# Kernel optimization log

Measured on AMD Instinct MI355X. Metric: run time of the kernel, lower is better.

The kernel has to match this reference:

```python
import jax, jax.numpy as jnp
import numpy as np

N_NODES = 100000
N_EDGES = 1250000
CH = [64, 64, 64]


def setup_inputs() -> dict:
    key = jax.random.key(0)
    ks = jax.random.split(key, 12)
    inp = {
        "x": jax.random.normal(ks[0], (N_NODES, CH[0]), dtype=jnp.float32),
        "edge_index": jax.random.randint(ks[1], (2, N_EDGES), 0, N_NODES, dtype=jnp.int64),
    }
    # Per-layer SAGEConv params (PyG default: out = lin_l(mean_aggr) + lin_r(x), bias only on lin_l)
    # plus per-channel PReLU weight (torch default init 0.25).
    for i in range(2):
        cin, cout = CH[i], CH[i + 1]
        s = 1.0 / np.sqrt(cin)
        inp[f"w_l{i}"] = jax.random.uniform(ks[2 + 4 * i], (cin, cout), jnp.float32, -s, s)
        inp[f"b_l{i}"] = jax.random.uniform(ks[3 + 4 * i], (cout,), jnp.float32, -s, s)
        inp[f"w_r{i}"] = jax.random.uniform(ks[4 + 4 * i], (cin, cout), jnp.float32, -s, s)
        inp[f"a{i}"] = jnp.full((cout,), 0.25, dtype=jnp.float32)
    return inp


def _sage_prelu(x, src, dst, w_l, b_l, w_r, a):
    n = x.shape[0]
    # mean aggregation of source features at destination nodes
    agg = jax.ops.segment_sum(x[src], dst, num_segments=n)  # [N, Cin]
    cnt = jax.ops.segment_sum(jnp.ones_like(dst, dtype=x.dtype), dst, num_segments=n)
    agg = agg / jnp.maximum(cnt, 1.0)[:, None]
    h = agg @ w_l + b_l + x @ w_r  # [N, Cout]
    return jnp.where(h >= 0, h, a * h)  # channel-wise PReLU


def reference(x, edge_index, w_l0, b_l0, w_r0, a0, w_l1, b_l1, w_r1, a1):
    src, dst = edge_index[0], edge_index[1]
    h = _sage_prelu(x, src, dst, w_l0, b_l0, w_r0, a0)
    h = _sage_prelu(h, src, dst, w_l1, b_l1, w_r1, a1)
    return h
```

## Files before the change

kernel.cpp:

```cpp
#include <hip/hip_runtime.h>
#include <hip/hip_fp16.h>

#define N_NODES 100000
#define N_EDGES 1250000
#define C 64
#define NPB 128
#define NB 782
#define CAP 2048
#define P1_CHUNKQ 2048
#define P1_BLOCKS 153
#define NQ (N_EDGES / 4)

typedef int vint4 __attribute__((ext_vector_type(4)));

__global__ __launch_bounds__(256) void partition_kernel(
        const int* __restrict__ src, const int* __restrict__ dst,
        int* __restrict__ gcnt, unsigned int* __restrict__ packed) {
    __shared__ int s_hist[4][NB];
    __shared__ int s_cur[NB];
    const int t = threadIdx.x;
    const int w = t >> 6;
    for (int i = t; i < 4 * NB; i += 256) ((int*)s_hist)[i] = 0;
    __syncthreads();

    const int qbase = blockIdx.x * P1_CHUNKQ;
    const vint4* d4 = (const vint4*)dst;
    const vint4* s4 = (const vint4*)src;

    vint4 dreg[8], sreg[8];
    bool val[8];
#pragma unroll
    for (int k = 0; k < 8; ++k) {
        int q = qbase + k * 256 + t;
        val[k] = q < NQ;
        if (val[k]) {
            dreg[k] = __builtin_nontemporal_load(&d4[q]);
            sreg[k] = __builtin_nontemporal_load(&s4[q]);
        }
    }

#pragma unroll
    for (int k = 0; k < 8; ++k) {
        if (val[k]) {
            atomicAdd(&s_hist[w][dreg[k].x >> 7], 1);
            atomicAdd(&s_hist[w][dreg[k].y >> 7], 1);
            atomicAdd(&s_hist[w][dreg[k].z >> 7], 1);
            atomicAdd(&s_hist[w][dreg[k].w >> 7], 1);
        }
    }
    __syncthreads();

    for (int b = t; b < NB; b += 256) {
        int tot = s_hist[0][b] + s_hist[1][b] + s_hist[2][b] + s_hist[3][b];
        s_cur[b] = (tot > 0) ? (b * CAP + atomicAdd(&gcnt[b], tot)) : 0;
    }
    __syncthreads();

#pragma unroll
    for (int k = 0; k < 8; ++k) {
        if (val[k]) {
            int bb, pos;
            bb = dreg[k].x >> 7; pos = atomicAdd(&s_cur[bb], 1);
            if (pos < (bb + 1) * CAP) packed[pos] = ((unsigned)sreg[k].x << 7) | (unsigned)(dreg[k].x & 127);
            bb = dreg[k].y >> 7; pos = atomicAdd(&s_cur[bb], 1);
            if (pos < (bb + 1) * CAP) packed[pos] = ((unsigned)sreg[k].y << 7) | (unsigned)(dreg[k].y & 127);
            bb = dreg[k].z >> 7; pos = atomicAdd(&s_cur[bb], 1);
            if (pos < (bb + 1) * CAP) packed[pos] = ((unsigned)sreg[k].z << 7) | (unsigned)(dreg[k].z & 127);
            bb = dreg[k].w >> 7; pos = atomicAdd(&s_cur[bb], 1);
            if (pos < (bb + 1) * CAP) packed[pos] = ((unsigned)sreg[k].w << 7) | (unsigned)(dreg[k].w & 127);
        }
    }
}

__global__ __launch_bounds__(256) void sort_kernel(
        const unsigned int* __restrict__ packed,
        const int* __restrict__ gcnt,
        int* __restrict__ offsets, int* __restrict__ sorted_src) {
    __shared__ int s_part[256];
    __shared__ unsigned int s_e[CAP];
    __shared__ int s_hist[NPB];
    __shared__ int s_excl[NPB];
    const int b = blockIdx.x;
    const int t = threadIdx.x;

    int psum = 0;
    for (int i = t; i < b; i += 256) psum += gcnt[i];
    s_part[t] = psum;
    __syncthreads();
    for (int off = 128; off > 0; off >>= 1) {
        if (t < off) s_part[t] += s_part[t + off];
        __syncthreads();
    }
    const int base = s_part[0];
    const int nb = min(gcnt[b], CAP);

    for (int i = t; i < NPB; i += 256) s_hist[i] = 0;
    __syncthreads();
    const vint4* p4 = (const vint4*)(packed + (size_t)b * CAP);
    for (int i4 = t; i4 * 4 < nb; i4 += 256) {
        vint4 u4 = __builtin_nontemporal_load(&p4[i4]);
        int i = i4 * 4;
        unsigned int u;
        u = (unsigned)u4.x; if (i + 0 < nb) { s_e[i + 0] = u; atomicAdd(&s_hist[u & 127u], 1); }
        u = (unsigned)u4.y; if (i + 1 < nb) { s_e[i + 1] = u; atomicAdd(&s_hist[u & 127u], 1); }
        u = (unsigned)u4.z; if (i + 2 < nb) { s_e[i + 2] = u; atomicAdd(&s_hist[u & 127u], 1); }
        u = (unsigned)u4.w; if (i + 3 < nb) { s_e[i + 3] = u; atomicAdd(&s_hist[u & 127u], 1); }
    }
    __syncthreads();
    if (t < NPB) s_excl[t] = s_hist[t];
    __syncthreads();
    for (int off = 1; off < NPB; off <<= 1) {
        int v = (t < NPB && t >= off) ? s_excl[t - off] : 0;
        __syncthreads();
        if (t < NPB) s_excl[t] += v;
        __syncthreads();
    }
    if (t < NPB) {
        int excl = s_excl[t] - s_hist[t];
        s_hist[t] = excl;
        int node = b * NPB + t;
        if (node < N_NODES) offsets[node] = base + excl;
    }
    __syncthreads();
    for (int i = t; i < nb; i += 256) {
        unsigned int u = s_e[i];
        int lp = atomicAdd(&s_hist[u & 127u], 1);
        sorted_src[base + lp] = (int)(u >> 7);
    }
    if (b == NB - 1 && t == 0) offsets[N_NODES] = N_EDGES;
}

template <typename XT>
__global__ __launch_bounds__(256) void dense_kernel(
        const XT* __restrict__ x,
        const float* __restrict__ wl, const float* __restrict__ wr,
        const float* __restrict__ bl,
        __half* __restrict__ z, __half* __restrict__ r, int n_nodes) {
    __shared__ float s_w[C][2 * C];
    __shared__ float s_x[64][C + 1];

    const int t = threadIdx.x;
    const int base = blockIdx.x * 64;

    for (int i = t; i < C * C; i += 256) {
        int k = i >> 6, c = i & 63;
        s_w[k][c] = wl[i];
        s_w[k][64 + c] = wr[i];
    }
    if constexpr (sizeof(XT) == 4) {
        for (int i = t; i < 1024; i += 256) {
            int n = i >> 4;
            int kq = i & 15;
            float4 v = make_float4(0.f, 0.f, 0.f, 0.f);
            if (base + n < n_nodes) v = ((const float4*)x)[((size_t)(base + n) << 4) + kq];
            s_x[n][kq * 4 + 0] = v.x;
            s_x[n][kq * 4 + 1] = v.y;
            s_x[n][kq * 4 + 2] = v.z;
            s_x[n][kq * 4 + 3] = v.w;
        }
    } else {
        for (int i = t; i < 2048; i += 256) {
            int n = i >> 5;
            int c2 = i & 31;
            float2 f = make_float2(0.f, 0.f);
            if (base + n < n_nodes)
                f = __half22float2(((const __half2*)x)[(size_t)(base + n) * 32 + c2]);
            s_x[n][2 * c2 + 0] = f.x;
            s_x[n][2 * c2 + 1] = f.y;
        }
    }
    __syncthreads();

    const int lane = t & 63;
    const int wv = t >> 6;
    const int cg = lane & 15;
    const int q = lane >> 4;
    const int n0 = wv * 16 + 4 * q;

    float4 bv = ((const float4*)bl)[cg];
    float accz[4][4];
    float accr[4][4];
#pragma unroll
    for (int i = 0; i < 4; ++i) {
        accz[i][0] = accz[i][1] = accz[i][2] = accz[i][3] = 0.f;
        accr[i][0] = bv.x; accr[i][1] = bv.y; accr[i][2] = bv.z; accr[i][3] = bv.w;
    }

#pragma unroll 8
    for (int k = 0; k < C; ++k) {
        float4 wlv = *(const float4*)&s_w[k][4 * cg];
        float4 wrv = *(const float4*)&s_w[k][64 + 4 * cg];
        float xk[4];
#pragma unroll
        for (int i = 0; i < 4; ++i) xk[i] = s_x[n0 + i][k];
#pragma unroll
        for (int i = 0; i < 4; ++i) {
            accz[i][0] += xk[i] * wlv.x;
            accz[i][1] += xk[i] * wlv.y;
            accz[i][2] += xk[i] * wlv.z;
            accz[i][3] += xk[i] * wlv.w;
            accr[i][0] += xk[i] * wrv.x;
            accr[i][1] += xk[i] * wrv.y;
            accr[i][2] += xk[i] * wrv.z;
            accr[i][3] += xk[i] * wrv.w;
        }
    }

#pragma unroll
    for (int i = 0; i < 4; ++i) {
        size_t gn = (size_t)base + n0 + i;
        if (gn < (size_t)n_nodes) {
            ((__half2*)z)[gn * 32 + 2 * cg + 0] = __float22half2_rn(make_float2(accz[i][0], accz[i][1]));
            ((__half2*)z)[gn * 32 + 2 * cg + 1] = __float22half2_rn(make_float2(accz[i][2], accz[i][3]));
            ((__half2*)r)[gn * 32 + 2 * cg + 0] = __float22half2_rn(make_float2(accr[i][0], accr[i][1]));
            ((__half2*)r)[gn * 32 + 2 * cg + 1] = __float22half2_rn(make_float2(accr[i][2], accr[i][3]));
        }
    }
}

template <typename OT>
__global__ __launch_bounds__(256) void gather_kernel(
        const __half* __restrict__ z,
        const __half* __restrict__ r,
        const int* __restrict__ offsets,
        const int* __restrict__ sorted_src,
        const float* __restrict__ a,
        OT* __restrict__ out) {
    const int lane = threadIdx.x & 63;
    const int c2 = lane & 31;
    const int sub = lane >> 5;
    const int node = (blockIdx.x << 3) + ((threadIdx.x >> 6) << 1) + sub;

    const int beg = offsets[node];
    const int deg = offsets[node + 1] - beg;
    const int last = deg - 1;
    const int* sp = sorted_src + beg;
    const unsigned int* z2 = (const unsigned int*)z;

    float2 acc = make_float2(0.f, 0.f);
    for (int j = 0; j < deg; j += 16) {
        int idx[16];
#pragma unroll
        for (int i = 0; i < 16; ++i)
            idx[i] = sp[min(j + i, last)];
        unsigned int v[16];
#pragma unroll
        for (int i = 0; i < 16; ++i)
            v[i] = z2[(size_t)idx[i] * 32 + c2];
#pragma unroll
        for (int i = 0; i < 16; ++i) {
            unsigned int uv = (j + i < deg) ? v[i] : 0u;
            float2 f = __half22float2(*(const __half2*)&uv);
            acc.x += f.x;
            acc.y += f.y;
        }
    }

    const float invd = 1.0f / (float)max(deg, 1);
    float2 rv = __half22float2(((const __half2*)r)[(size_t)node * 32 + c2]);
    float hx = acc.x * invd + rv.x;
    float hy = acc.y * invd + rv.y;
    float2 av = ((const float2*)a)[c2];
    float ox = hx >= 0.0f ? hx : av.x * hx;
    float oy = hy >= 0.0f ? hy : av.y * hy;
    if constexpr (sizeof(OT) == 2) {
        ((__half2*)out)[(size_t)node * 32 + c2] = __float22half2_rn(make_float2(ox, oy));
    } else {
        ((float2*)out)[(size_t)node * 32 + c2] = make_float2(ox, oy);
    }
}

extern "C" void kernel_launch(void* const* d_in, const int* in_sizes, int n_in,
                              void* d_out, int out_size, void* d_ws, size_t ws_size,
                              hipStream_t stream) {
    const float* x    = (const float*)d_in[0];
    const int*   ei   = (const int*)d_in[1];
    const float* w_l0 = (const float*)d_in[2];
    const float* b_l0 = (const float*)d_in[3];
    const float* w_r0 = (const float*)d_in[4];
    const float* a0   = (const float*)d_in[5];
    const float* w_l1 = (const float*)d_in[6];
    const float* b_l1 = (const float*)d_in[7];
    const float* w_r1 = (const float*)d_in[8];
    const float* a1   = (const float*)d_in[9];
    float* out = (float*)d_out;

    const int* src = ei;
    const int* dst = ei + N_EDGES;

    int* gcnt            = (int*)d_ws;
    int* offsets         = gcnt + 1024;
    unsigned int* packed = (unsigned int*)(offsets + (N_NODES + 1));
    int* sorted_src      = (int*)(packed + (size_t)NB * CAP);
    __half* Z            = (__half*)(sorted_src + N_EDGES);
    __half* R            = Z + (size_t)N_NODES * C;
    __half* H            = R + (size_t)N_NODES * C;

    hipMemsetAsync(gcnt, 0, 1024 * sizeof(int), stream);

    const int dblocks = (N_NODES + 63) / 64;
    const int nblocks = N_NODES / 8;

    partition_kernel<<<P1_BLOCKS, 256, 0, stream>>>(src, dst, gcnt, packed);
    sort_kernel<<<NB, 256, 0, stream>>>(packed, gcnt, offsets, sorted_src);

    dense_kernel<float><<<dblocks, 256, 0, stream>>>(x, w_l0, w_r0, b_l0, Z, R, N_NODES);
    gather_kernel<__half><<<nblocks, 256, 0, stream>>>(Z, R, offsets, sorted_src, a0, H);

    dense_kernel<__half><<<dblocks, 256, 0, stream>>>(H, w_l1, w_r1, b_l1, Z, R, N_NODES);
    gather_kernel<float><<<nblocks, 256, 0, stream>>>(Z, R, offsets, sorted_src, a1, out);
}
```

Baseline: 255.3 us.

## Use fp16 MFMA for dense transform and shrink partition chunks

Replaces the scalar FP32 FMA dense kernel with a matrix-core version. Inputs and weights are converted to fp16 in LDS and the 64x128 product is computed with mfma_f32_16x16x32_f16. Results are staged through LDS so they can be written out with coalesced 16-byte stores. Separately, the partition kernel now uses smaller chunks across more blocks to raise parallelism. The trade-off is that x and the weights are rounded to fp16 before the multiply, which lowers precision, and the extra blocks add more global atomics on the bucket counters.

```diff
diff --git a/kernel.cpp b/kernel.cpp
--- a/kernel.cpp
+++ b/kernel.cpp
@@ -7,11 +7,13 @@
 #define NPB 128
 #define NB 782
 #define CAP 2048
-#define P1_CHUNKQ 2048
-#define P1_BLOCKS 153
+#define P1_CHUNKQ 512
+#define P1_BLOCKS 611
 #define NQ (N_EDGES / 4)
 
 typedef int vint4 __attribute__((ext_vector_type(4)));
+typedef _Float16 f16x8 __attribute__((ext_vector_type(8)));
+typedef float f32x4 __attribute__((ext_vector_type(4)));
 
 __global__ __launch_bounds__(256) void partition_kernel(
         const int* __restrict__ src, const int* __restrict__ dst,
@@ -27,10 +29,10 @@
     const vint4* d4 = (const vint4*)dst;
     const vint4* s4 = (const vint4*)src;
 
-    vint4 dreg[8], sreg[8];
-    bool val[8];
-#pragma unroll
-    for (int k = 0; k < 8; ++k) {
+    vint4 dreg[2], sreg[2];
+    bool val[2];
+#pragma unroll
+    for (int k = 0; k < 2; ++k) {
         int q = qbase + k * 256 + t;
         val[k] = q < NQ;
         if (val[k]) {
@@ -40,7 +42,7 @@
     }
 
 #pragma unroll
-    for (int k = 0; k < 8; ++k) {
+    for (int k = 0; k < 2; ++k) {
         if (val[k]) {
             atomicAdd(&s_hist[w][dreg[k].x >> 7], 1);
             atomicAdd(&s_hist[w][dreg[k].y >> 7], 1);
@@ -57,7 +59,7 @@
     __syncthreads();
 
 #pragma unroll
-    for (int k = 0; k < 8; ++k) {
+    for (int k = 0; k < 2; ++k) {
         if (val[k]) {
             int bb, pos;
             bb = dreg[k].x >> 7; pos = atomicAdd(&s_cur[bb], 1);
@@ -130,90 +132,90 @@
     if (b == NB - 1 && t == 0) offsets[N_NODES] = N_EDGES;
 }
 
+#define AK 72
+#define OP 136
+
 template <typename XT>
-__global__ __launch_bounds__(256) void dense_kernel(
+__global__ __launch_bounds__(256) void dense_mfma_kernel(
         const XT* __restrict__ x,
         const float* __restrict__ wl, const float* __restrict__ wr,
         const float* __restrict__ bl,
         __half* __restrict__ z, __half* __restrict__ r, int n_nodes) {
-    __shared__ float s_w[C][2 * C];
-    __shared__ float s_x[64][C + 1];
+    __shared__ __align__(16) _Float16 smem[64 * AK + 128 * AK];
+    _Float16* s_a = smem;
+    _Float16* s_b = smem + 64 * AK;
+    _Float16* s_o = smem;
 
     const int t = threadIdx.x;
     const int base = blockIdx.x * 64;
 
-    for (int i = t; i < C * C; i += 256) {
-        int k = i >> 6, c = i & 63;
-        s_w[k][c] = wl[i];
-        s_w[k][64 + c] = wr[i];
+    for (int i = t; i < 4096; i += 256) {
+        int k = i >> 6, n = i & 63;
+        float vl = wl[i], vr = wr[i];
+        s_b[n * AK + k]        = (_Float16)vl;
+        s_b[(64 + n) * AK + k] = (_Float16)vr;
     }
     if constexpr (sizeof(XT) == 4) {
         for (int i = t; i < 1024; i += 256) {
-            int n = i >> 4;
-            int kq = i & 15;
+            int n = i >> 4, kq = i & 15;
             float4 v = make_float4(0.f, 0.f, 0.f, 0.f);
-            if (base + n < n_nodes) v = ((const float4*)x)[((size_t)(base + n) << 4) + kq];
-            s_x[n][kq * 4 + 0] = v.x;
-            s_x[n][kq * 4 + 1] = v.y;
-            s_x[n][kq * 4 + 2] = v.z;
-            s_x[n][kq * 4 + 3] = v.w;
+            if (base + n < n_nodes) v = ((const float4*)x)[(size_t)(base + n) * 16 + kq];
+            _Float16* p = &s_a[n * AK + kq * 4];
+            p[0] = (_Float16)v.x; p[1] = (_Float16)v.y;
+            p[2] = (_Float16)v.z; p[3] = (_Float16)v.w;
         }
     } else {
-        for (int i = t; i < 2048; i += 256) {
-            int n = i >> 5;
-            int c2 = i & 31;
-            float2 f = make_float2(0.f, 0.f);
-            if (base + n < n_nodes)
-                f = __half22float2(((const __half2*)x)[(size_t)(base + n) * 32 + c2]);
-            s_x[n][2 * c2 + 0] = f.x;
-            s_x[n][2 * c2 + 1] = f.y;
+        for (int i = t; i < 1024; i += 256) {
+            int n = i >> 4, kq = i & 15;
+            uint2 v = make_uint2(0u, 0u);
+            if (base + n < n_nodes) v = ((const uint2*)x)[(size_t)(base + n) * 16 + kq];
+            *(uint2*)&s_a[n * AK + kq * 4] = v;
         }
     }
     __syncthreads();
 
     const int lane = t & 63;
-    const int wv = t >> 6;
-    const int cg = lane & 15;
-    const int q = lane >> 4;
-    const int n0 = wv * 16 + 4 * q;
-
-    float4 bv = ((const float4*)bl)[cg];
-    float accz[4][4];
-    float accr[4][4];
-#pragma unroll
-    for (int i = 0; i < 4; ++i) {
-        accz[i][0] = accz[i][1] = accz[i][2] = accz[i][3] = 0.f;
-        accr[i][0] = bv.x; accr[i][1] = bv.y; accr[i][2] = bv.z; accr[i][3] = bv.w;
-    }
-
-#pragma unroll 8
-    for (int k = 0; k < C; ++k) {
-        float4 wlv = *(const float4*)&s_w[k][4 * cg];
-        float4 wrv = *(const float4*)&s_w[k][64 + 4 * cg];
-        float xk[4];
-#pragma unroll
-        for (int i = 0; i < 4; ++i) xk[i] = s_x[n0 + i][k];
-#pragma unroll
-        for (int i = 0; i < 4; ++i) {
-            accz[i][0] += xk[i] * wlv.x;
-            accz[i][1] += xk[i] * wlv.y;
-            accz[i][2] += xk[i] * wlv.z;
-            accz[i][3] += xk[i] * wlv.w;
-            accr[i][0] += xk[i] * wrv.x;
-            accr[i][1] += xk[i] * wrv.y;
-            accr[i][2] += xk[i] * wrv.z;
-            accr[i][3] += xk[i] * wrv.w;
-        }
-    }
-
-#pragma unroll
-    for (int i = 0; i < 4; ++i) {
-        size_t gn = (size_t)base + n0 + i;
+    const int w = t >> 6;
+    const int mrow = w * 16 + (lane & 15);
+    const int kg = (lane >> 4) * 8;
+    const int cb = lane & 15;
+
+    f16x8 a0 = *(const f16x8*)&s_a[mrow * AK + kg];
+    f16x8 a1 = *(const f16x8*)&s_a[mrow * AK + 32 + kg];
+    f32x4 acc[8];
+#pragma unroll
+    for (int nt = 0; nt < 8; ++nt) {
+        int col = nt * 16 + cb;
+        f16x8 b0 = *(const f16x8*)&s_b[col * AK + kg];
+        f16x8 b1 = *(const f16x8*)&s_b[col * AK + 32 + kg];
+        f32x4 c = {0.f, 0.f, 0.f, 0.f};
+        c = __builtin_amdgcn_mfma_f32_16x16x32_f16(a0, b0, c, 0, 0, 0);
+        c = __builtin_amdgcn_mfma_f32_16x16x32_f16(a1, b1, c, 0, 0, 0);
+        acc[nt] = c;
+    }
+    __syncthreads();
+
+#pragma unroll
+    for (int nt = 0; nt < 8; ++nt) {
+        int col = nt * 16 + cb;
+        float bias = (nt >= 4) ? bl[col - 64] : 0.0f;
+#pragma unroll
+        for (int j = 0; j < 4; ++j) {
+            int row = w * 16 + (lane >> 4) * 4 + j;
+            s_o[row * OP + col] = (_Float16)(acc[nt][j] + bias);
+        }
+    }
+    __syncthreads();
+
+    {
+        int row = t >> 2, q = t & 3;
+        size_t gn = (size_t)base + row;
         if (gn < (size_t)n_nodes) {
-            ((__half2*)z)[gn * 32 + 2 * cg + 0] = __float22half2_rn(make_float2(accz[i][0], accz[i][1]));
-            ((__half2*)z)[gn * 32 + 2 * cg + 1] = __float22half2_rn(make_float2(accz[i][2], accz[i][3]));
-            ((__half2*)r)[gn * 32 + 2 * cg + 0] = __float22half2_rn(make_float2(accr[i][0], accr[i][1]));
-            ((__half2*)r)[gn * 32 + 2 * cg + 1] = __float22half2_rn(make_float2(accr[i][2], accr[i][3]));
+            const uint4* sp = (const uint4*)&s_o[row * OP + q * 32];
+            __half* dp = (q < 2) ? (z + gn * 64 + q * 32) : (r + gn * 64 + (q - 2) * 32);
+#pragma unroll
+            for (int j = 0; j < 4; ++j)
+                ((uint4*)dp)[j] = sp[j];
         }
     }
 }
@@ -304,9 +306,9 @@
     partition_kernel<<<P1_BLOCKS, 256, 0, stream>>>(src, dst, gcnt, packed);
     sort_kernel<<<NB, 256, 0, stream>>>(packed, gcnt, offsets, sorted_src);
 
-    dense_kernel<float><<<dblocks, 256, 0, stream>>>(x, w_l0, w_r0, b_l0, Z, R, N_NODES);
+    dense_mfma_kernel<float><<<dblocks, 256, 0, stream>>>(x, w_l0, w_r0, b_l0, Z, R, N_NODES);
     gather_kernel<__half><<<nblocks, 256, 0, stream>>>(Z, R, offsets, sorted_src, a0, H);
 
-    dense_kernel<__half><<<dblocks, 256, 0, stream>>>(H, w_l1, w_r1, b_l1, Z, R, N_NODES);
+    dense_mfma_kernel<__half><<<dblocks, 256, 0, stream>>>(H, w_l1, w_r1, b_l1, Z, R, N_NODES);
     gather_kernel<float><<<nblocks, 256, 0, stream>>>(Z, R, offsets, sorted_src, a1, out);
 }
```

Result: faster. 242.9 us (-4.9%).
